# Performance work log

Measured on AMD Instinct MI355X. Metric: run time of the kernel, lower is better.

The kernel has to match this reference:

```python
import jax, jax.numpy as jnp
import numpy as np

B, T, D_MODEL, N_HEADS = 2, 2048, 1024, 16
HEAD_DIM = D_MODEL // N_HEADS
EPS = 1e-6
ROPE_BASE = 10000.0


def _rope_cos_sin(seq_len, dim, offset=0, dtype=jnp.float32):
    half = dim // 2
    inv_freq = 1.0 / (ROPE_BASE ** (jnp.arange(half, dtype=jnp.float32) / half))
    pos = jnp.arange(offset, offset + seq_len, dtype=jnp.float32)
    freqs = pos[:, None] * inv_freq[None, :]              # (T, half)
    emb = jnp.concatenate([freqs, freqs], axis=-1)        # (T, dim)
    return jnp.cos(emb).astype(dtype), jnp.sin(emb).astype(dtype)


def _rotate_half(x):
    x1, x2 = jnp.split(x, 2, axis=-1)
    return jnp.concatenate([-x2, x1], axis=-1)


def setup_inputs() -> dict:
    key = jax.random.key(0)
    k1, k2, k3 = jax.random.split(key, 3)
    x = jax.random.normal(k1, (B, T, D_MODEL), dtype=jnp.float32)
    norm_w = jnp.ones((D_MODEL,), dtype=jnp.float32)
    w_qkv = jax.random.normal(k2, (3 * D_MODEL, D_MODEL), dtype=jnp.float32) * 0.02
    w_out = jax.random.normal(k3, (D_MODEL, D_MODEL), dtype=jnp.float32) * 0.02
    return {"x": x, "norm_w": norm_w, "w_qkv": w_qkv, "w_out": w_out}


def reference(x, norm_w, w_qkv, w_out):
    # RMSNorm (pre-norm)
    h = x * jax.lax.rsqrt(jnp.mean(jnp.square(x), axis=-1, keepdims=True) + EPS) * norm_w
    # Fused QKV projection: (B,T,3*D)
    qkv = jnp.einsum('btd,ed->bte', h, w_qkv).reshape(B, T, 3, N_HEADS, HEAD_DIM)
    q, k, v = qkv[:, :, 0], qkv[:, :, 1], qkv[:, :, 2]   # each (B,T,H,Dh)
    # RoPE on q, k (offset=0)
    cos, sin = _rope_cos_sin(T, HEAD_DIM, dtype=q.dtype)
    cos = cos[None, :, None, :]
    sin = sin[None, :, None, :]
    q = q * cos + _rotate_half(q) * sin
    k = k * cos + _rotate_half(k) * sin
    # Causal scaled dot-product attention
    scale = 1.0 / np.sqrt(HEAD_DIM)
    scores = jnp.einsum('bqhd,bkhd->bhqk', q, k) * scale  # (B,H,T,T)
    causal = jnp.tril(jnp.ones((T, T), dtype=bool))
    scores = jnp.where(causal[None, None], scores, jnp.finfo(scores.dtype).min)
    attn = jax.nn.softmax(scores, axis=-1)
    out = jnp.einsum('bhqk,bkhd->bqhd', attn, v).reshape(B, T, D_MODEL)
    out = jnp.einsum('btd,ed->bte', out, w_out)
    return x + out
```

## Files before the change

kernel.cpp:

```cpp
#include <hip/hip_runtime.h>
#include <math.h>

typedef unsigned short u16;
typedef unsigned int u32;
typedef __attribute__((ext_vector_type(4))) float f32x4;
typedef __attribute__((ext_vector_type(8))) short s16x8;

#define GLL16(g, l) __builtin_amdgcn_global_load_lds( \
    (const __attribute__((address_space(1))) void*)(g), \
    (__attribute__((address_space(3))) void*)(l), 16, 0, 0)

#define MFMA16(a, b, c) __builtin_amdgcn_mfma_f32_16x16x32_bf16(a, b, c, 0, 0, 0)

__device__ __forceinline__ u16 f2bf(float f) {
  union { float f; u32 u; } v; v.f = f;
  u32 r = v.u + 0x7FFFu + ((v.u >> 16) & 1u);
  return (u16)(r >> 16);
}
__device__ __forceinline__ float bf2f(u16 h) {
  union { u32 u; float f; } v; v.u = ((u32)h) << 16;
  return v.f;
}
__device__ __forceinline__ u32 pk2bf(float lo, float hi) {
  union { float f; u32 u; } a, b; a.f = lo; b.f = hi;
  return __builtin_amdgcn_perm(b.u + 0x8000u, a.u + 0x8000u, 0x07060302u);
}
__device__ __forceinline__ float fexp2(float x) {
#if __has_builtin(__builtin_amdgcn_exp2f)
  return __builtin_amdgcn_exp2f(x);
#else
  return exp2f(x);
#endif
}
__device__ __forceinline__ float fsin_rev(float r) {
#if __has_builtin(__builtin_amdgcn_sinf)
  return __builtin_amdgcn_sinf(r);
#else
  return __sinf(r * 6.283185307179586f);
#endif
}
__device__ __forceinline__ float fcos_rev(float r) {
#if __has_builtin(__builtin_amdgcn_cosf)
  return __builtin_amdgcn_cosf(r);
#else
  return __cosf(r * 6.283185307179586f);
#endif
}

__global__ __launch_bounds__(256) void prep_kernel(const float* __restrict__ x,
                                                   const float* __restrict__ wgt,
                                                   const float* __restrict__ w_qkv,
                                                   const float* __restrict__ w_out,
                                                   u16* __restrict__ h,
                                                   u16* __restrict__ wqkv_b,
                                                   u16* __restrict__ wout_b) {
  __shared__ float red[4];
  const int bid = blockIdx.x, tid = threadIdx.x;
  if (bid < 4096) {
    const int row = bid;
    const float4 v = *(const float4*)&x[(size_t)row * 1024 + tid * 4];
    float ss = v.x * v.x + v.y * v.y + v.z * v.z + v.w * v.w;
    ss += __shfl_xor(ss, 1);  ss += __shfl_xor(ss, 2);  ss += __shfl_xor(ss, 4);
    ss += __shfl_xor(ss, 8);  ss += __shfl_xor(ss, 16); ss += __shfl_xor(ss, 32);
    if ((tid & 63) == 0) red[tid >> 6] = ss;
    __syncthreads();
    const float tot = red[0] + red[1] + red[2] + red[3];
    const float s = rsqrtf(tot * (1.0f / 1024.0f) + 1e-6f);
    const float4 g = *(const float4*)&wgt[tid * 4];
    uint2 o;
    o.x = (u32)f2bf(v.x * s * g.x) | ((u32)f2bf(v.y * s * g.y) << 16);
    o.y = (u32)f2bf(v.z * s * g.z) | ((u32)f2bf(v.w * s * g.w) << 16);
    *(uint2*)&h[(size_t)row * 1024 + tid * 4] = o;
  } else if (bid < 7168) {
    int i = (bid - 4096) * 256 + tid;
    float4 v = ((const float4*)w_qkv)[i];
    uint2 o;
    o.x = (u32)f2bf(v.x) | ((u32)f2bf(v.y) << 16);
    o.y = (u32)f2bf(v.z) | ((u32)f2bf(v.w) << 16);
    ((uint2*)wqkv_b)[i] = o;
  } else {
    int i = (bid - 7168) * 256 + tid;
    float4 v = ((const float4*)w_out)[i];
    uint2 o;
    o.x = (u32)f2bf(v.x) | ((u32)f2bf(v.y) << 16);
    o.y = (u32)f2bf(v.z) | ((u32)f2bf(v.w) << 16);
    ((uint2*)wout_b)[i] = o;
  }
}

template <int EPI>
__global__ __launch_bounds__(256) void gemm_bt(const u16* __restrict__ A,
                                               const u16* __restrict__ Bt,
                                               u16* __restrict__ Cb,
                                               float* __restrict__ Cf,
                                               const float* __restrict__ resid,
                                               int M, int N, int K) {
  __shared__ __attribute__((aligned(16))) u16 As[128 * 32];
  __shared__ __attribute__((aligned(16))) u16 Bs[128 * 32];
  const int tid = threadIdx.x;
  const int w = tid >> 6, lane = tid & 63;
  const int quad = lane >> 4, l16 = lane & 15;
  const int gm0 = blockIdx.y * 128, gn0 = blockIdx.x * 128;
  const int wm = (w & 1) * 64, wn = (w >> 1) * 64;

  f32x4 acc[4][4] = {};

  for (int k0 = 0; k0 < K; k0 += 32) {
    __syncthreads();
    if (w < 2) {
      #pragma unroll
      for (int i = 0; i < 4; ++i) {
        int sb = (w * 4 + i) * 64;
        int slot = sb + lane;
        int m = slot >> 2, c = (slot & 3) ^ (m & 3);
        GLL16(A + (size_t)(gm0 + m) * K + k0 + c * 8, &As[sb * 8]);
      }
    } else {
      #pragma unroll
      for (int i = 0; i < 4; ++i) {
        int sb = ((w - 2) * 4 + i) * 64;
        int slot = sb + lane;
        int n = slot >> 2, c = (slot & 3) ^ (n & 3);
        GLL16(Bt + (size_t)(gn0 + n) * K + k0 + c * 8, &Bs[sb * 8]);
      }
    }
    __syncthreads();
    s16x8 aF[4], bF[4];
    #pragma unroll
    for (int i = 0; i < 4; ++i) {
      int m = wm + i * 16 + l16;
      aF[i] = *(const s16x8*)&As[(m * 4 + (quad ^ (m & 3))) * 8];
    }
    #pragma unroll
    for (int j = 0; j < 4; ++j) {
      int n = wn + j * 16 + l16;
      bF[j] = *(const s16x8*)&Bs[(n * 4 + (quad ^ (n & 3))) * 8];
    }
    #pragma unroll
    for (int i = 0; i < 4; ++i)
      #pragma unroll
      for (int j = 0; j < 4; ++j)
        acc[i][j] = MFMA16(aF[i], bF[j], acc[i][j]);
  }

  #pragma unroll
  for (int i = 0; i < 4; ++i) {
    int row0 = gm0 + wm + i * 16 + quad * 4;
    #pragma unroll
    for (int j = 0; j < 4; ++j) {
      int col = gn0 + wn + j * 16 + l16;
      #pragma unroll
      for (int r = 0; r < 4; ++r) {
        size_t idx = (size_t)(row0 + r) * N + col;
        if (EPI == 0) Cb[idx] = f2bf(acc[i][j][r]);
        else          Cf[idx] = acc[i][j][r] + resid[idx];
      }
    }
  }
}

__global__ __launch_bounds__(512, 2) void gemm256(const u16* __restrict__ A,
                                                  const u16* __restrict__ Bt,
                                                  u16* __restrict__ Qr,
                                                  u16* __restrict__ Kr,
                                                  u16* __restrict__ Vt) {
  __shared__ __attribute__((aligned(16))) char smem[131072];
  const int tid = threadIdx.x;
  const int w = tid >> 6, lane = tid & 63;
  const int quad = lane >> 4, l16 = lane & 15;
  const int wr = w >> 2, wc = w & 3;
  const int rsw = l16 & 7;
  const int id = blockIdx.x;
  const int sw = (id & 7) * 24 + (id >> 3);
  const int by = sw / 12, bx = sw - by * 12;
  const int gm0 = by * 256, gn0 = bx * 256;
  const int scg = (lane & 7) ^ (lane >> 3);

  auto STAGE_HALF = [&](int kt, int part) {
    const int sb = (kt & 1) * 65536 + (part >> 1) * 32768 + (part & 1) * 16384;
    const u16* src = (part >> 1) ? Bt : A;
    const int g0 = ((part >> 1) ? gn0 : gm0) + (part & 1) * 128;
    const int k0 = kt * 64;
    #pragma unroll
    for (int q = 0; q < 2; ++q) {
      int r = q * 64 + (tid >> 3);
      GLL16(src + (size_t)(g0 + r) * 1024 + k0 + scg * 8,
            smem + sb + q * 8192 + w * 1024);
    }
  };

  f32x4 acc[8][4] = {};

  STAGE_HALF(0, 0); STAGE_HALF(0, 1);
  STAGE_HALF(0, 2); STAGE_HALF(0, 3);
  STAGE_HALF(1, 2); STAGE_HALF(1, 3);
  asm volatile("s_waitcnt vmcnt(4)" ::: "memory");
  __builtin_amdgcn_s_barrier();

  for (int kt = 0; kt < 16; ++kt) {
    const char* Ab = smem + (kt & 1) * 65536;
    const char* Bb = Ab + 32768;
    const int arow = wr * 128 + l16;
    const int brow = wc * 64 + l16;
    s16x8 aA[4][2], bB[4][2];

    #pragma unroll
    for (int fi = 0; fi < 4; ++fi) {
      const char* p = Ab + (arow + fi * 16) * 128;
      aA[fi][0] = *(const s16x8*)(p + ((quad ^ rsw) * 16));
      aA[fi][1] = *(const s16x8*)(p + (((4 + quad) ^ rsw) * 16));
    }
    #pragma unroll
    for (int fj = 0; fj < 4; ++fj) {
      const char* p = Bb + (brow + fj * 16) * 128;
      bB[fj][0] = *(const s16x8*)(p + ((quad ^ rsw) * 16));
      bB[fj][1] = *(const s16x8*)(p + (((4 + quad) ^ rsw) * 16));
    }

    if (kt < 15) { STAGE_HALF(kt + 1, 0); STAGE_HALF(kt + 1, 1); }

    __builtin_amdgcn_s_setprio(1);
    #pragma unroll
    for (int fi = 0; fi < 4; ++fi)
      #pragma unroll
      for (int fj = 0; fj < 4; ++fj) {
        acc[fi][fj] = MFMA16(aA[fi][0], bB[fj][0], acc[fi][fj]);
        acc[fi][fj] = MFMA16(aA[fi][1], bB[fj][1], acc[fi][fj]);
      }
    __builtin_amdgcn_s_setprio(0);

    #pragma unroll
    for (int fi = 0; fi < 4; ++fi) {
      const char* p = Ab + (arow + (4 + fi) * 16) * 128;
      aA[fi][0] = *(const s16x8*)(p + ((quad ^ rsw) * 16));
      aA[fi][1] = *(const s16x8*)(p + (((4 + quad) ^ rsw) * 16));
    }

    __builtin_amdgcn_s_setprio(1);
    #pragma unroll
    for (int fi = 0; fi < 4; ++fi)
      #pragma unroll
      for (int fj = 0; fj < 4; ++fj) {
        acc[4 + fi][fj] = MFMA16(aA[fi][0], bB[fj][0], acc[4 + fi][fj]);
        acc[4 + fi][fj] = MFMA16(aA[fi][1], bB[fj][1], acc[4 + fi][fj]);
      }
    __builtin_amdgcn_s_setprio(0);

    __builtin_amdgcn_s_barrier();

    if (kt < 14) {
      STAGE_HALF(kt + 2, 2); STAGE_HALF(kt + 2, 3);
      asm volatile("s_waitcnt vmcnt(4)" ::: "memory");
    } else if (kt == 14) {
      asm volatile("s_waitcnt vmcnt(0)" ::: "memory");
    }
    __builtin_amdgcn_s_barrier();
  }

  const int bb = gm0 >> 11;
  const int tt0 = (gm0 & 2047) + wr * 128;
  if (bx < 8) {
    const bool isQ = (bx < 4);
    const int h = ((bx & 3) << 2) + wc;
    const size_t obase = (size_t)(bb * 16 + h) * (2048 * 64);
    u16* dst = isQ ? Qr : Kr;
    const float SC = isQ ? 0.125f * 1.4426950408889634f : 1.0f;
    #pragma unroll
    for (int fj = 0; fj < 2; ++fj) {
      const int jj = fj * 16 + l16;
      const float invf_rev = fexp2(-(float)jj * (13.287712379549449f / 32.0f)) *
                             0.15915494309189535f;
      #pragma unroll
      for (int g = 0; g < 8; ++g) {
        #pragma unroll
        for (int r = 0; r < 4; ++r) {
          const int t = tt0 + g * 16 + quad * 4 + r;
          const float rev = (float)t * invf_rev;
          const float fr = rev - floorf(rev);
          const float sn = fsin_rev(fr), cs = fcos_rev(fr);
          const float q1 = acc[g][fj][r], q2 = acc[g][2 + fj][r];
          dst[obase + (size_t)t * 64 + jj]      = f2bf((q1 * cs - q2 * sn) * SC);
          dst[obase + (size_t)t * 64 + jj + 32] = f2bf((q2 * cs + q1 * sn) * SC);
        }
      }
    }
  } else {
    const int h = ((bx - 8) << 2) + wc;
    const size_t obase = (size_t)(bb * 16 + h) * 64;
    u16* Vl = (u16*)smem + wc * 16384;
    #pragma unroll
    for (int g = 0; g < 8; ++g)
      #pragma unroll
      for (int fj = 0; fj < 4; ++fj) {
        const int d = fj * 16 + l16;
        #pragma unroll
        for (int r = 0; r < 4; ++r) {
          const int tl = wr * 128 + g * 16 + quad * 4 + r;
          Vl[tl * 64 + (d ^ (((tl >> 3) & 7) << 3))] = f2bf(acc[g][fj][r]);
        }
      }
    __syncthreads();
    const int c = lane & 7, lg = lane >> 3;
    const int tb = gm0 & 2047;
    #pragma unroll
    for (int c32 = wr * 2; c32 < wr * 2 + 2; ++c32)
      #pragma unroll
      for (int dp = 0; dp < 8; ++dp) {
        const int d = dp * 8 + lg;
        const u16* col = Vl + (c32 * 64 + c * 8) * 64 + (d ^ (c << 3));
        u16 tmp[8];
        #pragma unroll
        for (int k = 0; k < 8; ++k) tmp[k] = col[k * 64];
        *(uint4*)&Vt[(obase + d) * 2048 + tb + c32 * 64 + c * 8] = *(uint4*)tmp;
      }
  }
}

__global__ __launch_bounds__(512, 2) void attn_kernel(const u16* __restrict__ Qr,
                                                      const u16* __restrict__ Kr,
                                                      const u16* __restrict__ Vt,
                                                      u16* __restrict__ AO) {
  __shared__ __attribute__((aligned(16))) char smem[102400];
  const int tid = threadIdx.x;
  const int w = tid >> 6, lane = tid & 63;
  const int wq = w & 3, wp = w >> 2;
  const int quad = lane >> 4, l16 = lane & 15;
  const int id = blockIdx.x;
  const int bh = id & 31;
  const int c  = id >> 5;
  const int b = bh >> 4, h = bh & 15;
  const size_t qkb = (size_t)bh * (2048 * 64);
  const size_t vtb = (size_t)bh * (64 * 2048);
  u16* Pw = (u16*)(smem + 65536 + w * 4608);

  const int srow = lane >> 3;
  const int scg  = (lane & 7) ^ srow;
  const int smat = w & 1, stp = (w >> 1) & 1, shalf = (w >> 2) & 1;

  auto STAGE = [&](int j0, int d) {
    const int jn = j0 + stp;
    if (smat == 0) {
      #pragma unroll
      for (int ii = 0; ii < 4; ++ii) {
        int i = shalf * 4 + ii;
        GLL16(Kr + qkb + (size_t)(jn * 64 + i * 8 + srow) * 64 + scg * 8,
              smem + (stp * 2 + d) * 8192 + i * 1024);
      }
    } else {
      #pragma unroll
      for (int ii = 0; ii < 4; ++ii) {
        int i = shalf * 4 + ii;
        GLL16(Vt + vtb + (size_t)(i * 8 + srow) * 2048 + jn * 64 + scg * 8,
              smem + 32768 + (stp * 2 + d) * 8192 + i * 1024);
      }
    }
  };

  for (int t = 0; t < 2; ++t) {
    const int qblk = t ? (15 - c) : c;
    const int q0w = qblk * 128 + wq * 32;
    const int steps = qblk + 1;

    s16x8 bQ[2][2];
    #pragma unroll
    for (int s = 0; s < 2; ++s)
      #pragma unroll
      for (int hf = 0; hf < 2; ++hf)
        bQ[s][hf] = *(const s16x8*)&Qr[qkb + (size_t)(q0w + s * 16 + l16) * 64 + hf * 32 + quad * 8];

    f32x4 O[2][4] = {};
    float l_run[2] = {0.0f, 0.0f};

    STAGE(0, 0);
    __syncthreads();

    for (int st = 0; st < steps; ++st) {
      const int cur = st & 1;
      if (st + 1 < steps) STAGE(2 * st + 2, cur ^ 1);

      const int j = 2 * st + wp;
      if (j * 64 <= q0w + 31) {
        const u16* Kb = (const u16*)(smem + (wp * 2 + cur) * 8192);
        const u16* Vb = (const u16*)(smem + 32768 + (wp * 2 + cur) * 8192);
        const bool masked = (j * 64 + 63 > q0w);
        const int rsw = (l16 & 7);

        s16x8 aK[4][2];
        #pragma unroll
        for (int kt = 0; kt < 4; ++kt)
          #pragma unroll
          for (int hf = 0; hf < 2; ++hf)
            aK[kt][hf] = *(const s16x8*)&Kb[(kt * 16 + l16) * 64 + (((hf * 4 + quad) ^ rsw) * 8)];

        f32x4 S[2][4];
        __builtin_amdgcn_s_setprio(1);
        #pragma unroll
        for (int kt = 0; kt < 4; ++kt)
          #pragma unroll
          for (int s = 0; s < 2; ++s) {
            f32x4 z = {};
            z = MFMA16(aK[kt][0], bQ[s][0], z);
            S[s][kt] = MFMA16(aK[kt][1], bQ[s][1], z);
          }
        __builtin_amdgcn_s_setprio(0);

        if (masked) {
          #pragma unroll
          for (int s = 0; s < 2; ++s) {
            int q = q0w + s * 16 + l16;
            #pragma unroll
            for (int kt = 0; kt < 4; ++kt) {
              int key0 = j * 64 + kt * 16 + quad * 4;
              #pragma unroll
              for (int r = 0; r < 4; ++r)
                if (key0 + r > q) S[s][kt][r] = -1e30f;
            }
          }
        }

        #pragma unroll
        for (int s = 0; s < 2; ++s) {
          float sum = 0.0f;
          #pragma unroll
          for (int kt = 0; kt < 4; ++kt) {
            #pragma unroll
            for (int r = 0; r < 4; ++r) {
              float e = fexp2(S[s][kt][r]);
              S[s][kt][r] = e;
              sum += e;
            }
          }
          sum += __shfl_xor(sum, 16);
          sum += __shfl_xor(sum, 32);
          l_run[s] += sum;
          #pragma unroll
          for (int kt = 0; kt < 4; ++kt) {
            uint2 pw;
            pw.x = pk2bf(S[s][kt][0], S[s][kt][1]);
            pw.y = pk2bf(S[s][kt][2], S[s][kt][3]);
            *(uint2*)&Pw[s * 1152 + l16 * 72 + kt * 16 + quad * 4] = pw;
          }
        }

        s16x8 bP[2][2];
        #pragma unroll
        for (int s = 0; s < 2; ++s) {
          bP[s][0] = *(const s16x8*)&Pw[s * 1152 + l16 * 72 + quad * 8];
          bP[s][1] = *(const s16x8*)&Pw[s * 1152 + l16 * 72 + 32 + quad * 8];
        }
        s16x8 aV[4][2];
        #pragma unroll
        for (int dt = 0; dt < 4; ++dt)
          #pragma unroll
          for (int hf = 0; hf < 2; ++hf)
            aV[dt][hf] = *(const s16x8*)&Vb[(dt * 16 + l16) * 64 + (((hf * 4 + quad) ^ rsw) * 8)];

        __builtin_amdgcn_s_setprio(1);
        #pragma unroll
        for (int dt = 0; dt < 4; ++dt)
          #pragma unroll
          for (int s = 0; s < 2; ++s) {
            O[s][dt] = MFMA16(aV[dt][0], bP[s][0], O[s][dt]);
            O[s][dt] = MFMA16(aV[dt][1], bP[s][1], O[s][dt]);
          }
        __builtin_amdgcn_s_setprio(0);
      }

      __syncthreads();
    }

    if (wp == 1) {
      float* Lsl = (float*)(smem + 65536 + wq * 512);
      Lsl[lane]      = l_run[0];
      Lsl[64 + lane] = l_run[1];
      f32x4* slot = (f32x4*)smem + wq * 512;
      #pragma unroll
      for (int s = 0; s < 2; ++s)
        #pragma unroll
        for (int dt = 0; dt < 4; ++dt)
          slot[(s * 4 + dt) * 64 + lane] = O[s][dt];
    }
    __syncthreads();
    if (wp == 0) {
      const float* Lsl = (const float*)(smem + 65536 + wq * 512);
      const f32x4* slot = (const f32x4*)smem + wq * 512;
      #pragma unroll
      for (int s = 0; s < 2; ++s) {
        float l_tot = l_run[s] + Lsl[s * 64 + lane];
        float inv = __builtin_amdgcn_rcpf(l_tot);
        int q = q0w + s * 16 + l16;
        #pragma unroll
        for (int dt = 0; dt < 4; ++dt) {
          f32x4 o = O[s][dt] + slot[(s * 4 + dt) * 64 + lane];
          uint2 ow;
          ow.x = pk2bf(o[0] * inv, o[1] * inv);
          ow.y = pk2bf(o[2] * inv, o[3] * inv);
          *(uint2*)&AO[(size_t)(b * 2048 + q) * 1024 + h * 64 + dt * 16 + quad * 4] = ow;
        }
      }
    }
    __syncthreads();
  }
}

extern "C" void kernel_launch(void* const* d_in, const int* in_sizes, int n_in,
                              void* d_out, int out_size, void* d_ws, size_t ws_size,
                              hipStream_t stream) {
  const float* x      = (const float*)d_in[0];
  const float* norm_w = (const float*)d_in[1];
  const float* w_qkv  = (const float*)d_in[2];
  const float* w_out  = (const float*)d_in[3];
  float* out = (float*)d_out;

  u16* ws     = (u16*)d_ws;
  u16* wqkv_b = ws;
  u16* wout_b = wqkv_b + 3145728;
  u16* h_b    = wout_b + 1048576;
  u16* Qr     = h_b + 4194304 + 12582912;
  u16* Kr     = Qr + 4194304;
  u16* Vt     = Kr + 4194304;
  u16* AO     = Vt + 4194304;

  prep_kernel<<<8192, 256, 0, stream>>>(x, norm_w, w_qkv, w_out, h_b, wqkv_b, wout_b);
  gemm256<<<192, 512, 0, stream>>>(h_b, wqkv_b, Qr, Kr, Vt);
  attn_kernel<<<256, 512, 0, stream>>>(Qr, Kr, Vt, AO);
  gemm_bt<1><<<dim3(8, 32), 256, 0, stream>>>(AO, wout_b, nullptr, out, x,
                                              4096, 1024, 1024);
}
```

Measured before the change: 175.3 us.

## Shrink attention blocks to 256 threads and drop K/V double buffering

The attention kernel now uses 4-wave blocks over 64-query tiles instead of 8-wave blocks over 128-query tiles, launching twice as many blocks. It halves shared memory to fit three blocks per CU. The K/V ping-pong buffering is removed: each step stages a tile and then synchronises. The aim is higher occupancy and finer load balance, at the cost of exposed load latency and an extra barrier every step.

```diff
diff --git a/kernel.cpp b/kernel.cpp
--- a/kernel.cpp
+++ b/kernel.cpp
@@ -316,14 +316,14 @@
   }
 }
 
-__global__ __launch_bounds__(512, 2) void attn_kernel(const u16* __restrict__ Qr,
+__global__ __launch_bounds__(256, 3) void attn_kernel(const u16* __restrict__ Qr,
                                                       const u16* __restrict__ Kr,
                                                       const u16* __restrict__ Vt,
                                                       u16* __restrict__ AO) {
-  __shared__ __attribute__((aligned(16))) char smem[102400];
+  __shared__ __attribute__((aligned(16))) char smem[51200];
   const int tid = threadIdx.x;
   const int w = tid >> 6, lane = tid & 63;
-  const int wq = w & 3, wp = w >> 2;
+  const int wq = w & 1, wp = w >> 1;
   const int quad = lane >> 4, l16 = lane & 15;
   const int id = blockIdx.x;
   const int bh = id & 31;
@@ -331,35 +331,31 @@
   const int b = bh >> 4, h = bh & 15;
   const size_t qkb = (size_t)bh * (2048 * 64);
   const size_t vtb = (size_t)bh * (64 * 2048);
-  u16* Pw = (u16*)(smem + 65536 + w * 4608);
+  u16* Pw = (u16*)(smem + 32768 + w * 4608);
 
   const int srow = lane >> 3;
   const int scg  = (lane & 7) ^ srow;
-  const int smat = w & 1, stp = (w >> 1) & 1, shalf = (w >> 2) & 1;
-
-  auto STAGE = [&](int j0, int d) {
-    const int jn = j0 + stp;
+  const int smat = w & 1, spar = w >> 1;
+
+  auto STAGE = [&](int st) {
+    const int jn = 2 * st + spar;
     if (smat == 0) {
       #pragma unroll
-      for (int ii = 0; ii < 4; ++ii) {
-        int i = shalf * 4 + ii;
+      for (int i = 0; i < 8; ++i)
         GLL16(Kr + qkb + (size_t)(jn * 64 + i * 8 + srow) * 64 + scg * 8,
-              smem + (stp * 2 + d) * 8192 + i * 1024);
-      }
+              smem + spar * 8192 + i * 1024);
     } else {
       #pragma unroll
-      for (int ii = 0; ii < 4; ++ii) {
-        int i = shalf * 4 + ii;
+      for (int i = 0; i < 8; ++i)
         GLL16(Vt + vtb + (size_t)(i * 8 + srow) * 2048 + jn * 64 + scg * 8,
-              smem + 32768 + (stp * 2 + d) * 8192 + i * 1024);
-      }
+              smem + 16384 + spar * 8192 + i * 1024);
     }
   };
 
   for (int t = 0; t < 2; ++t) {
-    const int qblk = t ? (15 - c) : c;
-    const int q0w = qblk * 128 + wq * 32;
-    const int steps = qblk + 1;
+    const int qi = t ? (31 - c) : c;
+    const int q0w = qi * 64 + wq * 32;
+    const int steps = (qi + 2) >> 1;
 
     s16x8 bQ[2][2];
     #pragma unroll
@@ -371,17 +367,14 @@
     f32x4 O[2][4] = {};
     float l_run[2] = {0.0f, 0.0f};
 
-    STAGE(0, 0);
-    __syncthreads();
-
     for (int st = 0; st < steps; ++st) {
-      const int cur = st & 1;
-      if (st + 1 < steps) STAGE(2 * st + 2, cur ^ 1);
+      STAGE(st);
+      __syncthreads();
 
       const int j = 2 * st + wp;
       if (j * 64 <= q0w + 31) {
-        const u16* Kb = (const u16*)(smem + (wp * 2 + cur) * 8192);
-        const u16* Vb = (const u16*)(smem + 32768 + (wp * 2 + cur) * 8192);
+        const u16* Kb = (const u16*)(smem + wp * 8192);
+        const u16* Vb = (const u16*)(smem + 16384 + wp * 8192);
         const bool masked = (j * 64 + 63 > q0w);
         const int rsw = (l16 & 7);
 
@@ -470,7 +463,7 @@
     }
 
     if (wp == 1) {
-      float* Lsl = (float*)(smem + 65536 + wq * 512);
+      float* Lsl = (float*)(smem + 16384 + wq * 512);
       Lsl[lane]      = l_run[0];
       Lsl[64 + lane] = l_run[1];
       f32x4* slot = (f32x4*)smem + wq * 512;
@@ -482,7 +475,7 @@
     }
     __syncthreads();
     if (wp == 0) {
-      const float* Lsl = (const float*)(smem + 65536 + wq * 512);
+      const float* Lsl = (const float*)(smem + 16384 + wq * 512);
       const f32x4* slot = (const f32x4*)smem + wq * 512;
       #pragma unroll
       for (int s = 0; s < 2; ++s) {
@@ -523,7 +516,7 @@
 
   prep_kernel<<<8192, 256, 0, stream>>>(x, norm_w, w_qkv, w_out, h_b, wqkv_b, wout_b);
   gemm256<<<192, 512, 0, stream>>>(h_b, wqkv_b, Qr, Kr, Vt);
-  attn_kernel<<<256, 512, 0, stream>>>(Qr, Kr, Vt, AO);
+  attn_kernel<<<512, 256, 0, stream>>>(Qr, Kr, Vt, AO);
   gemm_bt<1><<<dim3(8, 32), 256, 0, stream>>>(AO, wout_b, nullptr, out, x,
                                               4096, 1024, 1024);
 }
```

New measurement: 178.6 us. About the same (+1.9%).

## Split attention blocks per query tile and shrink LDS to raise occupancy

Applied to the files above, without the earlier changes.

Each attention block now handles one query block instead of looping over a paired light and heavy query block. The grid doubles to 512 blocks, with adjacent block ids pairing short and long causal rows. The P staging buffer shrinks to 2 KB per wave with an XOR swizzle, and P is written and read one sub-tile at a time. This cuts LDS from 100 KB to 80 KB and the launch bound now asks for higher occupancy, so more blocks can run per CU and latency is better hidden. The cost is less work per block for amortising the Q load and the epilogue, possible register spills under the tighter launch bound, and heavy and light blocks may no longer balance out.

```diff
diff --git a/kernel.cpp b/kernel.cpp
--- a/kernel.cpp
+++ b/kernel.cpp
@@ -316,22 +316,24 @@
   }
 }
 
-__global__ __launch_bounds__(512, 2) void attn_kernel(const u16* __restrict__ Qr,
+__global__ __launch_bounds__(512, 4) void attn_kernel(const u16* __restrict__ Qr,
                                                       const u16* __restrict__ Kr,
                                                       const u16* __restrict__ Vt,
                                                       u16* __restrict__ AO) {
-  __shared__ __attribute__((aligned(16))) char smem[102400];
+  __shared__ __attribute__((aligned(16))) char smem[81920];
   const int tid = threadIdx.x;
   const int w = tid >> 6, lane = tid & 63;
   const int wq = w & 3, wp = w >> 2;
   const int quad = lane >> 4, l16 = lane & 15;
   const int id = blockIdx.x;
-  const int bh = id & 31;
-  const int c  = id >> 5;
+  const int kk = id >> 1, odd = id & 1;
+  const int bh = kk & 31;
+  const int qh = kk >> 5;
+  const int qblk = odd ? (15 - qh) : qh;
   const int b = bh >> 4, h = bh & 15;
   const size_t qkb = (size_t)bh * (2048 * 64);
   const size_t vtb = (size_t)bh * (64 * 2048);
-  u16* Pw = (u16*)(smem + 65536 + w * 4608);
+  char* PwB = smem + 65536 + w * 2048;
 
   const int srow = lane >> 3;
   const int scg  = (lane & 7) ^ srow;
@@ -356,150 +358,140 @@
     }
   };
 
-  for (int t = 0; t < 2; ++t) {
-    const int qblk = t ? (15 - c) : c;
-    const int q0w = qblk * 128 + wq * 32;
-    const int steps = qblk + 1;
-
-    s16x8 bQ[2][2];
-    #pragma unroll
-    for (int s = 0; s < 2; ++s)
-      #pragma unroll
-      for (int hf = 0; hf < 2; ++hf)
-        bQ[s][hf] = *(const s16x8*)&Qr[qkb + (size_t)(q0w + s * 16 + l16) * 64 + hf * 32 + quad * 8];
-
-    f32x4 O[2][4] = {};
-    float l_run[2] = {0.0f, 0.0f};
-
-    STAGE(0, 0);
-    __syncthreads();
-
-    for (int st = 0; st < steps; ++st) {
-      const int cur = st & 1;
-      if (st + 1 < steps) STAGE(2 * st + 2, cur ^ 1);
-
-      const int j = 2 * st + wp;
-      if (j * 64 <= q0w + 31) {
-        const u16* Kb = (const u16*)(smem + (wp * 2 + cur) * 8192);
-        const u16* Vb = (const u16*)(smem + 32768 + (wp * 2 + cur) * 8192);
-        const bool masked = (j * 64 + 63 > q0w);
-        const int rsw = (l16 & 7);
-
-        s16x8 aK[4][2];
-        #pragma unroll
-        for (int kt = 0; kt < 4; ++kt)
-          #pragma unroll
-          for (int hf = 0; hf < 2; ++hf)
-            aK[kt][hf] = *(const s16x8*)&Kb[(kt * 16 + l16) * 64 + (((hf * 4 + quad) ^ rsw) * 8)];
-
-        f32x4 S[2][4];
-        __builtin_amdgcn_s_setprio(1);
-        #pragma unroll
-        for (int kt = 0; kt < 4; ++kt)
-          #pragma unroll
-          for (int s = 0; s < 2; ++s) {
-            f32x4 z = {};
-            z = MFMA16(aK[kt][0], bQ[s][0], z);
-            S[s][kt] = MFMA16(aK[kt][1], bQ[s][1], z);
-          }
-        __builtin_amdgcn_s_setprio(0);
-
-        if (masked) {
-          #pragma unroll
-          for (int s = 0; s < 2; ++s) {
-            int q = q0w + s * 16 + l16;
-            #pragma unroll
-            for (int kt = 0; kt < 4; ++kt) {
-              int key0 = j * 64 + kt * 16 + quad * 4;
-              #pragma unroll
-              for (int r = 0; r < 4; ++r)
-                if (key0 + r > q) S[s][kt][r] = -1e30f;
-            }
-          }
-        }
-
+  const int q0w = qblk * 128 + wq * 32;
+  const int steps = qblk + 1;
+
+  s16x8 bQ[2][2];
+  #pragma unroll
+  for (int s = 0; s < 2; ++s)
+    #pragma unroll
+    for (int hf = 0; hf < 2; ++hf)
+      bQ[s][hf] = *(const s16x8*)&Qr[qkb + (size_t)(q0w + s * 16 + l16) * 64 + hf * 32 + quad * 8];
+
+  f32x4 O[2][4] = {};
+  float l_run[2] = {0.0f, 0.0f};
+
+  STAGE(0, 0);
+  __syncthreads();
+
+  for (int st = 0; st < steps; ++st) {
+    const int cur = st & 1;
+    if (st + 1 < steps) STAGE(2 * st + 2, cur ^ 1);
+
+    const int j = 2 * st + wp;
+    if (j * 64 <= q0w + 31) {
+      const u16* Kb = (const u16*)(smem + (wp * 2 + cur) * 8192);
+      const u16* Vb = (const u16*)(smem + 32768 + (wp * 2 + cur) * 8192);
+      const bool masked = (j * 64 + 63 > q0w);
+      const int rsw = (l16 & 7);
+
+      s16x8 aK[4][2];
+      #pragma unroll
+      for (int kt = 0; kt < 4; ++kt)
+        #pragma unroll
+        for (int hf = 0; hf < 2; ++hf)
+          aK[kt][hf] = *(const s16x8*)&Kb[(kt * 16 + l16) * 64 + (((hf * 4 + quad) ^ rsw) * 8)];
+
+      f32x4 S[2][4];
+      __builtin_amdgcn_s_setprio(1);
+      #pragma unroll
+      for (int kt = 0; kt < 4; ++kt)
         #pragma unroll
         for (int s = 0; s < 2; ++s) {
-          float sum = 0.0f;
+          f32x4 z = {};
+          z = MFMA16(aK[kt][0], bQ[s][0], z);
+          S[s][kt] = MFMA16(aK[kt][1], bQ[s][1], z);
+        }
+      __builtin_amdgcn_s_setprio(0);
+
+      if (masked) {
+        #pragma unroll
+        for (int s = 0; s < 2; ++s) {
+          int q = q0w + s * 16 + l16;
           #pragma unroll
           for (int kt = 0; kt < 4; ++kt) {
+            int key0 = j * 64 + kt * 16 + quad * 4;
             #pragma unroll
-            for (int r = 0; r < 4; ++r) {
-              float e = fexp2(S[s][kt][r]);
-              S[s][kt][r] = e;
-              sum += e;
-            }
+            for (int r = 0; r < 4; ++r)
+              if (key0 + r > q) S[s][kt][r] = -1e30f;
           }
-          sum += __shfl_xor(sum, 16);
-          sum += __shfl_xor(sum, 32);
-          l_run[s] += sum;
+        }
+      }
+
+      s16x8 aV[4][2];
+      #pragma unroll
+      for (int s = 0; s < 2; ++s) {
+        float sum = 0.0f;
+        #pragma unroll
+        for (int kt = 0; kt < 4; ++kt) {
           #pragma unroll
-          for (int kt = 0; kt < 4; ++kt) {
-            uint2 pw;
-            pw.x = pk2bf(S[s][kt][0], S[s][kt][1]);
-            pw.y = pk2bf(S[s][kt][2], S[s][kt][3]);
-            *(uint2*)&Pw[s * 1152 + l16 * 72 + kt * 16 + quad * 4] = pw;
+          for (int r = 0; r < 4; ++r) {
+            float e = fexp2(S[s][kt][r]);
+            S[s][kt][r] = e;
+            sum += e;
           }
         }
-
-        s16x8 bP[2][2];
-        #pragma unroll
-        for (int s = 0; s < 2; ++s) {
-          bP[s][0] = *(const s16x8*)&Pw[s * 1152 + l16 * 72 + quad * 8];
-          bP[s][1] = *(const s16x8*)&Pw[s * 1152 + l16 * 72 + 32 + quad * 8];
-        }
-        s16x8 aV[4][2];
-        #pragma unroll
-        for (int dt = 0; dt < 4; ++dt)
+        sum += __shfl_xor(sum, 16);
+        sum += __shfl_xor(sum, 32);
+        l_run[s] += sum;
+        #pragma unroll
+        for (int kt = 0; kt < 4; ++kt) {
+          uint2 pw;
+          pw.x = pk2bf(S[s][kt][0], S[s][kt][1]);
+          pw.y = pk2bf(S[s][kt][2], S[s][kt][3]);
+          *(uint2*)&PwB[l16 * 128 + (((2 * kt + (quad >> 1)) ^ rsw) * 16) + (quad & 1) * 8] = pw;
+        }
+        if (s == 0) {
           #pragma unroll
-          for (int hf = 0; hf < 2; ++hf)
-            aV[dt][hf] = *(const s16x8*)&Vb[(dt * 16 + l16) * 64 + (((hf * 4 + quad) ^ rsw) * 8)];
-
+          for (int dt = 0; dt < 4; ++dt)
+            #pragma unroll
+            for (int hf = 0; hf < 2; ++hf)
+              aV[dt][hf] = *(const s16x8*)&Vb[(dt * 16 + l16) * 64 + (((hf * 4 + quad) ^ rsw) * 8)];
+        }
+        s16x8 bP0 = *(const s16x8*)&PwB[l16 * 128 + ((quad ^ rsw) * 16)];
+        s16x8 bP1 = *(const s16x8*)&PwB[l16 * 128 + (((4 + quad) ^ rsw) * 16)];
         __builtin_amdgcn_s_setprio(1);
         #pragma unroll
-        for (int dt = 0; dt < 4; ++dt)
-          #pragma unroll
-          for (int s = 0; s < 2; ++s) {
-            O[s][dt] = MFMA16(aV[dt][0], bP[s][0], O[s][dt]);
-            O[s][dt] = MFMA16(aV[dt][1], bP[s][1], O[s][dt]);
-          }
+        for (int dt = 0; dt < 4; ++dt) {
+          O[s][dt] = MFMA16(aV[dt][0], bP0, O[s][dt]);
+          O[s][dt] = MFMA16(aV[dt][1], bP1, O[s][dt]);
+        }
         __builtin_amdgcn_s_setprio(0);
       }
-
-      __syncthreads();
-    }
-
-    if (wp == 1) {
-      float* Lsl = (float*)(smem + 65536 + wq * 512);
-      Lsl[lane]      = l_run[0];
-      Lsl[64 + lane] = l_run[1];
-      f32x4* slot = (f32x4*)smem + wq * 512;
-      #pragma unroll
-      for (int s = 0; s < 2; ++s)
-        #pragma unroll
-        for (int dt = 0; dt < 4; ++dt)
-          slot[(s * 4 + dt) * 64 + lane] = O[s][dt];
-    }
+    }
+
     __syncthreads();
-    if (wp == 0) {
-      const float* Lsl = (const float*)(smem + 65536 + wq * 512);
-      const f32x4* slot = (const f32x4*)smem + wq * 512;
-      #pragma unroll
-      for (int s = 0; s < 2; ++s) {
-        float l_tot = l_run[s] + Lsl[s * 64 + lane];
-        float inv = __builtin_amdgcn_rcpf(l_tot);
-        int q = q0w + s * 16 + l16;
-        #pragma unroll
-        for (int dt = 0; dt < 4; ++dt) {
-          f32x4 o = O[s][dt] + slot[(s * 4 + dt) * 64 + lane];
-          uint2 ow;
-          ow.x = pk2bf(o[0] * inv, o[1] * inv);
-          ow.y = pk2bf(o[2] * inv, o[3] * inv);
-          *(uint2*)&AO[(size_t)(b * 2048 + q) * 1024 + h * 64 + dt * 16 + quad * 4] = ow;
-        }
-      }
-    }
-    __syncthreads();
+  }
+
+  if (wp == 1) {
+    float* Lsl = (float*)(smem + 65536 + wq * 512);
+    Lsl[lane]      = l_run[0];
+    Lsl[64 + lane] = l_run[1];
+    f32x4* slot = (f32x4*)smem + wq * 512;
+    #pragma unroll
+    for (int s = 0; s < 2; ++s)
+      #pragma unroll
+      for (int dt = 0; dt < 4; ++dt)
+        slot[(s * 4 + dt) * 64 + lane] = O[s][dt];
+  }
+  __syncthreads();
+  if (wp == 0) {
+    const float* Lsl = (const float*)(smem + 65536 + wq * 512);
+    const f32x4* slot = (const f32x4*)smem + wq * 512;
+    #pragma unroll
+    for (int s = 0; s < 2; ++s) {
+      float l_tot = l_run[s] + Lsl[s * 64 + lane];
+      float inv = __builtin_amdgcn_rcpf(l_tot);
+      int q = q0w + s * 16 + l16;
+      #pragma unroll
+      for (int dt = 0; dt < 4; ++dt) {
+        f32x4 o = O[s][dt] + slot[(s * 4 + dt) * 64 + lane];
+        uint2 ow;
+        ow.x = pk2bf(o[0] * inv, o[1] * inv);
+        ow.y = pk2bf(o[2] * inv, o[3] * inv);
+        *(uint2*)&AO[(size_t)(b * 2048 + q) * 1024 + h * 64 + dt * 16 + quad * 4] = ow;
+      }
+    }
   }
 }
 
@@ -523,7 +515,7 @@
 
   prep_kernel<<<8192, 256, 0, stream>>>(x, norm_w, w_qkv, w_out, h_b, wqkv_b, wout_b);
   gemm256<<<192, 512, 0, stream>>>(h_b, wqkv_b, Qr, Kr, Vt);
-  attn_kernel<<<256, 512, 0, stream>>>(Qr, Kr, Vt, AO);
+  attn_kernel<<<512, 512, 0, stream>>>(Qr, Kr, Vt, AO);
   gemm_bt<1><<<dim3(8, 32), 256, 0, stream>>>(AO, wout_b, nullptr, out, x,
                                               4096, 1024, 1024);
 }
```

Result: slower. 281.0 us (+60.3%).
